# Optimization experiments

Hardware: AMD Instinct MI355X
Metric: run time of the kernel (lower is better)

Reference implementation:

```python
import jax, jax.numpy as jnp
import numpy as np

NUM_MODELS = 16
NUM_CLASSES = 17929
HIDDEN = 4
BATCH = 512


def setup_inputs() -> dict:
    key = jax.random.key(0)
    k1, k2, k3, k4, k5 = jax.random.split(key, 5)
    x = jax.random.normal(k1, (NUM_MODELS, BATCH, NUM_CLASSES), dtype=jnp.float32)
    # stacked per-class Linear(num_models, hidden) weights/biases
    W1 = jax.random.normal(k2, (NUM_CLASSES, HIDDEN, NUM_MODELS), dtype=jnp.float32) * 0.1
    b1 = jax.random.normal(k3, (NUM_CLASSES, HIDDEN), dtype=jnp.float32) * 0.1
    # stacked per-class Linear(hidden, 1) weights (squeezed) / biases
    W2 = jax.random.normal(k4, (NUM_CLASSES, HIDDEN), dtype=jnp.float32) * 0.1
    b2 = jax.random.normal(k5, (NUM_CLASSES,), dtype=jnp.float32) * 0.1
    return {"x": x, "W1": W1, "b1": b1, "W2": W2, "b2": b2}


def reference(x, W1, b1, W2, b2):
    # x: [M, B, C] -> permute(1, 2, 0) -> [B, C, M]
    xp = jnp.transpose(x, (1, 2, 0))
    # per-class first Linear + ReLU: h[b,c,h] = relu(sum_m xp[b,c,m] * W1[c,h,m] + b1[c,h])
    h = jax.nn.relu(jnp.einsum('bcm,chm->bch', xp, W1) + b1[None, :, :])
    # per-class second Linear(hidden -> 1), concatenated over classes -> [B, C]
    out = jnp.einsum('bch,ch->bc', h, W2) + b2[None, :]
    return out
```

## Files before the change

kernel.cpp:

```cpp
#include <hip/hip_runtime.h>


#define NUM_MODELS 16
#define HIDDEN 4
#define BATCH 512
#define NUM_CLASSES 17929
#define KB 16
#define CT 256

typedef __attribute__((address_space(1))) const void as1_void;
typedef __attribute__((address_space(3))) void as3_void;

__global__ __launch_bounds__(CT) void FamilyMLPLinear_kernel(
    const float* __restrict__ x,
    const float* __restrict__ W1,
    const float* __restrict__ b1,
    const float* __restrict__ W2,
    const float* __restrict__ b2,
    float* __restrict__ out)
{
    __shared__ float xs[NUM_MODELS][CT];

    const int t  = threadIdx.x;
    const int c0 = blockIdx.x * CT;
    const int b0 = blockIdx.y * KB;
    const int c  = c0 + t;
    const int cw = (c < NUM_CLASSES) ? c : (NUM_CLASSES - 1);

    float w1[HIDDEN][NUM_MODELS];
    const float4* W1v = (const float4*)(W1 + (size_t)cw * (HIDDEN * NUM_MODELS));
    #pragma unroll
    for (int j = 0; j < HIDDEN; ++j) {
        #pragma unroll
        for (int q = 0; q < NUM_MODELS / 4; ++q) {
            float4 v = W1v[j * (NUM_MODELS / 4) + q];
            w1[j][q * 4 + 0] = v.x;
            w1[j][q * 4 + 1] = v.y;
            w1[j][q * 4 + 2] = v.z;
            w1[j][q * 4 + 3] = v.w;
        }
    }
    const float4 b1v = *(const float4*)(b1 + (size_t)cw * HIDDEN);
    const float bias1[HIDDEN] = {b1v.x, b1v.y, b1v.z, b1v.w};
    const float4 w2v = *(const float4*)(W2 + (size_t)cw * HIDDEN);
    const float w2[HIDDEN] = {w2v.x, w2v.y, w2v.z, w2v.w};
    const float bias2 = b2[cw];

    const size_t BC = (size_t)BATCH * NUM_CLASSES;

    if (c0 + CT <= NUM_CLASSES) {
        const int lane = t & 63;
        const int wv   = t >> 6;

        #pragma unroll 1
        for (int bi = 0; bi < KB; ++bi) {
            const int b = b0 + bi;
            const size_t row0 = (size_t)b * NUM_CLASSES + c0;
            const int   sb  = (int)(row0 & 3);
            const size_t A0 = row0 - (size_t)sb;

            #pragma unroll
            for (int r = 0; r < 4; ++r) {
                const int m = wv * 4 + r;
                const float* gp = x + (size_t)m * BC + A0 + (size_t)(lane << 2);
                __builtin_amdgcn_global_load_lds((as1_void*)gp, (as3_void*)&xs[m][0],
                                                 16, 0, 0);
            }
            __syncthreads();

            float xv[NUM_MODELS];
            const int ti = t + sb;
            if (ti < CT) {
                #pragma unroll
                for (int m = 0; m < NUM_MODELS; ++m) xv[m] = xs[m][ti];
            } else {
                const float* xp = x + row0 + t;
                #pragma unroll
                for (int m = 0; m < NUM_MODELS; ++m) xv[m] = xp[(size_t)m * BC];
            }

            float acc = bias2;
            #pragma unroll
            for (int j = 0; j < HIDDEN; ++j) {
                float h = bias1[j];
                #pragma unroll
                for (int m = 0; m < NUM_MODELS; ++m)
                    h = fmaf(xv[m], w1[j][m], h);
                h = fmaxf(h, 0.0f);
                acc = fmaf(h, w2[j], acc);
            }
            __builtin_nontemporal_store(acc, out + (size_t)b * NUM_CLASSES + c);
            __syncthreads();
        }
    } else {
        if (c < NUM_CLASSES) {
            #pragma unroll 1
            for (int bi = 0; bi < KB; ++bi) {
                const int b = b0 + bi;
                const float* xp = x + (size_t)b * NUM_CLASSES + c;
                float xv[NUM_MODELS];
                #pragma unroll
                for (int m = 0; m < NUM_MODELS; ++m)
                    xv[m] = xp[(size_t)m * BC];
                float acc = bias2;
                #pragma unroll
                for (int j = 0; j < HIDDEN; ++j) {
                    float h = bias1[j];
                    #pragma unroll
                    for (int m = 0; m < NUM_MODELS; ++m)
                        h = fmaf(xv[m], w1[j][m], h);
                    h = fmaxf(h, 0.0f);
                    acc = fmaf(h, w2[j], acc);
                }
                out[(size_t)b * NUM_CLASSES + c] = acc;
            }
        }
    }
}

extern "C" void kernel_launch(void* const* d_in, const int* in_sizes, int n_in,
                              void* d_out, int out_size, void* d_ws, size_t ws_size,
                              hipStream_t stream) {
    const float* x  = (const float*)d_in[0];
    const float* W1 = (const float*)d_in[1];
    const float* b1 = (const float*)d_in[2];
    const float* W2 = (const float*)d_in[3];
    const float* b2 = (const float*)d_in[4];
    float* out = (float*)d_out;

    dim3 grid((NUM_CLASSES + CT - 1) / CT, BATCH / KB);
    FamilyMLPLinear_kernel<<<grid, CT, 0, stream>>>(x, W1, b1, W2, b2, out);
}
```

Measured before the change: 812.1 us.

## Double-buffer LDS staging of x with async loads and padded rows

Converts the per-batch-row LDS staging into a two-buffer pipeline. The next row's async global-to-LDS loads are issued before the current row is computed, with explicit vmcnt waits and barriers so loads overlap compute. Each staged row is padded by four extra elements loaded with 4-byte async loads, which removes the unaligned-tail fallback that read x straight from global memory. In exchange it doubles LDS use and relies on hand-counted vmcnt values, which break if the number of memory operations per iteration changes.

```diff
diff --git a/kernel.cpp b/kernel.cpp
--- a/kernel.cpp
+++ b/kernel.cpp
@@ -7,9 +7,13 @@
 #define NUM_CLASSES 17929
 #define KB 16
 #define CT 256
+#define ROWPAD 264
 
 typedef __attribute__((address_space(1))) const void as1_void;
 typedef __attribute__((address_space(3))) void as3_void;
+
+#define ASM_VMCNT(n) asm volatile("s_waitcnt vmcnt(" #n ")" ::: "memory")
+#define ASM_BARRIER() asm volatile("s_barrier" ::: "memory")
 
 __global__ __launch_bounds__(CT) void FamilyMLPLinear_kernel(
     const float* __restrict__ x,
@@ -19,13 +23,15 @@
     const float* __restrict__ b2,
     float* __restrict__ out)
 {
-    __shared__ float xs[NUM_MODELS][CT];
+    __shared__ float xs[2][NUM_MODELS][ROWPAD];
 
-    const int t  = threadIdx.x;
-    const int c0 = blockIdx.x * CT;
-    const int b0 = blockIdx.y * KB;
-    const int c  = c0 + t;
-    const int cw = (c < NUM_CLASSES) ? c : (NUM_CLASSES - 1);
+    const int t    = threadIdx.x;
+    const int lane = t & 63;
+    const int wv   = t >> 6;
+    const int c0   = blockIdx.x * CT;
+    const int b0   = blockIdx.y * KB;
+    const int c    = c0 + t;
+    const int cw   = (c < NUM_CLASSES) ? c : (NUM_CLASSES - 1);
 
     float w1[HIDDEN][NUM_MODELS];
     const float4* W1v = (const float4*)(W1 + (size_t)cw * (HIDDEN * NUM_MODELS));
@@ -49,36 +55,34 @@
     const size_t BC = (size_t)BATCH * NUM_CLASSES;
 
     if (c0 + CT <= NUM_CLASSES) {
-        const int lane = t & 63;
-        const int wv   = t >> 6;
 
-        #pragma unroll 1
-        for (int bi = 0; bi < KB; ++bi) {
-            const int b = b0 + bi;
+        auto stage = [&](int buf, int b) {
             const size_t row0 = (size_t)b * NUM_CLASSES + c0;
-            const int   sb  = (int)(row0 & 3);
-            const size_t A0 = row0 - (size_t)sb;
-
+            const size_t A0   = row0 & ~(size_t)3;
             #pragma unroll
             for (int r = 0; r < 4; ++r) {
                 const int m = wv * 4 + r;
                 const float* gp = x + (size_t)m * BC + A0 + (size_t)(lane << 2);
-                __builtin_amdgcn_global_load_lds((as1_void*)gp, (as3_void*)&xs[m][0],
-                                                 16, 0, 0);
+                __builtin_amdgcn_global_load_lds((as1_void*)gp,
+                                                 (as3_void*)&xs[buf][m][0], 16, 0, 0);
             }
-            __syncthreads();
+            if (lane < 4) {
+                #pragma unroll
+                for (int r = 0; r < 4; ++r) {
+                    const int m = wv * 4 + r;
+                    const float* gp2 = x + (size_t)m * BC + A0 + 256 + (size_t)lane;
+                    __builtin_amdgcn_global_load_lds((as1_void*)gp2,
+                                                     (as3_void*)&xs[buf][m][256], 4, 0, 0);
+                }
+            }
+        };
 
+        auto computeStore = [&](int buf, int b) {
+            const int ti = t + (b & 3);
             float xv[NUM_MODELS];
-            const int ti = t + sb;
-            if (ti < CT) {
-                #pragma unroll
-                for (int m = 0; m < NUM_MODELS; ++m) xv[m] = xs[m][ti];
-            } else {
-                const float* xp = x + row0 + t;
-                #pragma unroll
-                for (int m = 0; m < NUM_MODELS; ++m) xv[m] = xp[(size_t)m * BC];
-            }
-
+            #pragma unroll
+            for (int m = 0; m < NUM_MODELS; ++m)
+                xv[m] = xs[buf][m][ti];
             float acc = bias2;
             #pragma unroll
             for (int j = 0; j < HIDDEN; ++j) {
@@ -90,8 +94,28 @@
                 acc = fmaf(h, w2[j], acc);
             }
             __builtin_nontemporal_store(acc, out + (size_t)b * NUM_CLASSES + c);
-            __syncthreads();
+        };
+
+        stage(0, b0);
+        ASM_VMCNT(0);
+        ASM_BARRIER();
+        __builtin_amdgcn_sched_barrier(0);
+
+        #pragma unroll 1
+        for (int bi = 0; bi < KB - 1; ++bi) {
+            stage((bi + 1) & 1, b0 + bi + 1);
+            ASM_VMCNT(9);
+            ASM_BARRIER();
+            __builtin_amdgcn_sched_barrier(0);
+            computeStore(bi & 1, b0 + bi);
+            __builtin_amdgcn_sched_barrier(0);
+            ASM_BARRIER();
         }
+
+        ASM_VMCNT(1);
+        ASM_BARRIER();
+        __builtin_amdgcn_sched_barrier(0);
+        computeStore((KB - 1) & 1, b0 + KB - 1);
     } else {
         if (c < NUM_CLASSES) {
             #pragma unroll 1
```

New measurement: 768.0 us. 1.06x faster.
